# Kernel optimization log

Measured on AMD Instinct MI355X. Metric: run time of the kernel, lower is better.

The kernel has to match this reference:

```python
import jax, jax.numpy as jnp
import numpy as np


def setup_inputs() -> dict:
    key = jax.random.key(0)
    kq, kk, kv = jax.random.split(key, 3)
    B, S, D = 32, 2048, 64  # (batch*heads, seq_len, head_dim)
    q = jax.random.normal(kq, (B, S, D), dtype=jnp.float32)
    k = jax.random.normal(kk, (B, S, D), dtype=jnp.float32)
    v = jax.random.normal(kv, (B, S, D), dtype=jnp.float32)
    return {"q": q, "k": k, "v": v}


def reference(q, k, v):
    # attention = q @ k^T  (no scale, no mask: defaults scale=None, attn_mask=None)
    scores = jnp.einsum("bqd,bkd->bqk", q, k)  # [B, S, S] materialized, as in source
    attn = jax.nn.softmax(scores, axis=2)      # Softmax(dim=2) == key axis for 3D
    # dropout is identity in eval / deterministic reference
    return jnp.einsum("bqk,bkd->bqd", attn, v)
```

## Files before the change

kernel.cpp:

```cpp
#include <hip/hip_runtime.h>
#include <stdint.h>

typedef __attribute__((ext_vector_type(4)))  float    f32x4;
typedef __attribute__((ext_vector_type(16))) float    f32x16;
typedef __attribute__((ext_vector_type(8)))  _Float16 f16x8;
typedef __attribute__((ext_vector_type(8)))  __bf16   bf16x8;

#define SEQ   2048
#define DH    64
#define BQ    128
#define BK    64
#define NT    (SEQ / BK)
#define ROWE  72
#define TILEE (64 * ROWE)
#define L2E   1.44269504088896340736f

#if __has_builtin(__builtin_amdgcn_exp2f)
static __device__ __forceinline__ float fast_exp2(float x) { return __builtin_amdgcn_exp2f(x); }
#else
static __device__ __forceinline__ float fast_exp2(float x) {
  float r; asm("v_exp_f32 %0, %1" : "=v"(r) : "v"(x)); return r;
}
#endif
static __device__ __forceinline__ uint32_t pack2_bf16(float a, float b) {
  union { __bf16 h[2]; uint32_t u; } cv;
  cv.h[0] = (__bf16)a; cv.h[1] = (__bf16)b;
  return cv.u;
}
union frag_u { uint32_t u[4]; bf16x8 v; };

typedef const __attribute__((address_space(1))) uint32_t* gp1_t;
typedef __attribute__((address_space(3))) uint32_t*       lp3_t;

__host__ __device__ inline int sigma32(int m) {
  int b = m & 3, h = (m >> 2) & 1, c = m >> 3;
  return ((c & 1) << 4) | (h << 3) | ((c >> 1) << 2) | b;
}

__global__ __launch_bounds__(256)
void prepass(const float* __restrict__ K, const float* __restrict__ V,
             _Float16* __restrict__ Kh, __bf16* __restrict__ Vh) {
  const int blk = blockIdx.x;
  const int tid = threadIdx.x;
  if (blk < 32 * NT) {
    const float* src = K + ((size_t)(blk >> 5) * SEQ + (size_t)(blk & 31) * 64) * DH;
    _Float16*    dst = Kh + (size_t)blk * TILEE;
    const int row = tid >> 2, c = (tid & 3) << 4;
    const int srow = (row & 32) | sigma32(row & 31);
    const float* sp = src + srow * DH + c;
    f32x4 x0 = *(const f32x4*)(sp + 0),  x1 = *(const f32x4*)(sp + 4);
    f32x4 x2 = *(const f32x4*)(sp + 8),  x3 = *(const f32x4*)(sp + 12);
    f16x8 h0, h1;
#pragma unroll
    for (int j = 0; j < 4; ++j) {
      h0[j] = (_Float16)x0[j]; h0[j + 4] = (_Float16)x1[j];
      h1[j] = (_Float16)x2[j]; h1[j + 4] = (_Float16)x3[j];
    }
    *(f16x8*)(dst + row * ROWE + c)     = h0;
    *(f16x8*)(dst + row * ROWE + c + 8) = h1;
  } else {
    const int blk2 = blk - 32 * NT;
    const float* src = V + ((size_t)(blk2 >> 5) * SEQ + (size_t)(blk2 & 31) * 64) * DH;
    __bf16*      dst = Vh + (size_t)blk2 * TILEE;
#pragma unroll
    for (int it = 0; it < 4; ++it) {
      int task = tid + it * 256;
      int d = task & 63, g = task >> 6;
      const float* sp = src + (size_t)(4 * g) * DH + d;
      __bf16 hv[4];
#pragma unroll
      for (int j = 0; j < 4; ++j) hv[j] = (__bf16)sp[(size_t)j * DH];
      *(uint64_t*)(dst + d * ROWE + 4 * g) = *(uint64_t*)hv;
    }
  }
}

__global__ __launch_bounds__(256, 2)
void flash_attn_v10(const float* __restrict__ Q, const _Float16* __restrict__ Kh,
                    const __bf16* __restrict__ Vh, float* __restrict__ O) {
  __shared__ _Float16 Ksb[2][64][ROWE];
  __shared__ __bf16   Vtb[2][64][ROWE];
  __shared__ float    Ls[4][32];

  const int tid  = threadIdx.x;
  const int wv   = tid >> 6;
  const int lane = tid & 63;
  const int hfw  = lane >> 5;
  const int l31  = lane & 31;

  const int batch = blockIdx.x & 31;
  const int qblk  = blockIdx.x >> 5;

  const float* Qb = Q + (size_t)batch * SEQ * DH;
  float*       Ob = O + (size_t)batch * SEQ * DH;
  const uint32_t* Kt0 = (const uint32_t*)(Kh + (size_t)batch * NT * TILEE);
  const uint32_t* Vt0 = (const uint32_t*)(Vh + (size_t)batch * NT * TILEE);

  auto stageK = [&](int t, int buf) {
    const uint32_t* kgp = Kt0 + (size_t)t * (TILEE / 2);
    lp3_t kl = (lp3_t)&Ksb[buf][0][0];
#pragma unroll
    for (int j = wv; j < 9; j += 4)
      __builtin_amdgcn_global_load_lds((gp1_t)(kgp + j * 256 + lane * 4), kl + j * 256, 16, 0, 0);
  };
  auto stageV = [&](int t, int buf) {
    const uint32_t* vgp = Vt0 + (size_t)t * (TILEE / 2);
    lp3_t vl = (lp3_t)&Vtb[buf][0][0];
#pragma unroll
    for (int j = wv; j < 9; j += 4)
      __builtin_amdgcn_global_load_lds((gp1_t)(vgp + j * 256 + lane * 4), vl + j * 256, 16, 0, 0);
  };

  const int qrow = qblk * BQ + wv * 32 + l31;
  f16x8 qf[4];
  {
    const float* qp = Qb + (size_t)qrow * DH + hfw * 8;
#pragma unroll
    for (int ks = 0; ks < 4; ++ks) {
      f32x4 a = *(const f32x4*)(qp + ks * 16);
      f32x4 b = *(const f32x4*)(qp + ks * 16 + 4);
#pragma unroll
      for (int j = 0; j < 4; ++j) {
        qf[ks][j]     = (_Float16)(a[j] * L2E);
        qf[ks][j + 4] = (_Float16)(b[j] * L2E);
      }
    }
  }

  f32x16 acc0 = {}, acc1 = {};
  float lsum = 0.f;

  auto qk = [&](int buf, f32x16& s0, f32x16& s1) {
    s0 = {}; s1 = {};
#pragma unroll
    for (int ks = 0; ks < 4; ++ks) {
      const int dof = ks * 16 + hfw * 8;
      f16x8 kf0 = *(const f16x8*)&Ksb[buf][l31][dof];
      f16x8 kf1 = *(const f16x8*)&Ksb[buf][l31 + 32][dof];
      s0 = __builtin_amdgcn_mfma_f32_32x32x16_f16(kf0, qf[ks], s0, 0, 0, 0);
      s1 = __builtin_amdgcn_mfma_f32_32x32x16_f16(kf1, qf[ks], s1, 0, 0, 0);
    }
  };

  auto step = [&](int i, f32x16& c0, f32x16& c1, f32x16& n0, f32x16& n1) {
    __syncthreads();
    if (i + 2 < NT) stageK(i + 2, i & 1);
    if (i + 1 < NT) stageV(i + 1, (i + 1) & 1);
    __builtin_amdgcn_s_setprio(1);

    if (i + 1 < NT) qk((i + 1) & 1, n0, n1);

    frag_u fr[4];
#pragma unroll
    for (int t2 = 0; t2 < 2; ++t2) {
      const f32x16& s = t2 ? c1 : c0;
      float p[16];
#pragma unroll
      for (int j = 0; j < 16; ++j) p[j] = fast_exp2(s[j]);
      float a0 = (p[0] + p[1]) + (p[2] + p[3]);
      float a1 = (p[4] + p[5]) + (p[6] + p[7]);
      float a2 = (p[8] + p[9]) + (p[10] + p[11]);
      float a3 = (p[12] + p[13]) + (p[14] + p[15]);
      lsum += (a0 + a1) + (a2 + a3);
      fr[2 * t2    ].u[0] = pack2_bf16(p[0],  p[1]);
      fr[2 * t2    ].u[1] = pack2_bf16(p[2],  p[3]);
      fr[2 * t2    ].u[2] = pack2_bf16(p[8],  p[9]);
      fr[2 * t2    ].u[3] = pack2_bf16(p[10], p[11]);
      fr[2 * t2 + 1].u[0] = pack2_bf16(p[4],  p[5]);
      fr[2 * t2 + 1].u[1] = pack2_bf16(p[6],  p[7]);
      fr[2 * t2 + 1].u[2] = pack2_bf16(p[12], p[13]);
      fr[2 * t2 + 1].u[3] = pack2_bf16(p[14], p[15]);
    }

    const int vb = i & 1;
#pragma unroll
    for (int ks = 0; ks < 4; ++ks) {
      const int kof = ks * 16 + hfw * 8;
      bf16x8 v0 = *(const bf16x8*)&Vtb[vb][l31][kof];
      bf16x8 v1 = *(const bf16x8*)&Vtb[vb][l31 + 32][kof];
      acc0 = __builtin_amdgcn_mfma_f32_32x32x16_bf16(fr[ks].v, v0, acc0, 0, 0, 0);
      acc1 = __builtin_amdgcn_mfma_f32_32x32x16_bf16(fr[ks].v, v1, acc1, 0, 0, 0);
    }
    __builtin_amdgcn_s_setprio(0);
  };

  stageK(0, 0); stageV(0, 0); stageK(1, 1);
  __syncthreads();
  f32x16 sA0, sA1, sB0, sB1;
  qk(0, sA0, sA1);

#pragma unroll 1
  for (int i = 0; i < NT; i += 2) {
    step(i,     sA0, sA1, sB0, sB1);
    step(i + 1, sB0, sB1, sA0, sA1);
  }

  float tot = lsum + __shfl_xor(lsum, 32);
  Ls[wv][l31] = __builtin_amdgcn_rcpf(tot);
#pragma unroll
  for (int j = 0; j < 16; ++j) {
    int row = (j & 3) + 8 * (j >> 2) + 4 * hfw;
    float inv = Ls[wv][row];
    size_t off = (size_t)(qblk * BQ + wv * 32 + row) * DH + l31;
    Ob[off]      = acc0[j] * inv;
    Ob[off + 32] = acc1[j] * inv;
  }
}

extern "C" void kernel_launch(void* const* d_in, const int* in_sizes, int n_in,
                              void* d_out, int out_size, void* d_ws, size_t ws_size,
                              hipStream_t stream) {
  (void)in_sizes; (void)n_in; (void)ws_size; (void)out_size;
  const float* q = (const float*)d_in[0];
  const float* k = (const float*)d_in[1];
  const float* v = (const float*)d_in[2];
  float* o = (float*)d_out;
  _Float16* Kh = (_Float16*)d_ws;
  __bf16*   Vh = (__bf16*)((char*)d_ws + (size_t)32 * NT * TILEE * sizeof(_Float16));

  prepass<<<dim3(2 * 32 * NT), dim3(256), 0, stream>>>(k, v, Kh, Vh);
  flash_attn_v10<<<dim3(32 * (SEQ / BQ)), dim3(256), 0, stream>>>(q, Kh, Vh, o);
}
```

Baseline: 138.6 us.

## Split key range across two warp groups per block with LDS reduction

Blocks grow to 512 threads: each of the four query warps is paired with a second warp that handles the second half of the key tiles (split-K within a block). The two halves keep their own double-buffered K/V tiles in LDS, and their partial outputs and row sums are combined through shared memory at the end. The software pipeline that overlapped the next tile's QK with the current tile's PV is dropped in favour of a simpler loop with setprio hints. The aim is more waves per CU to hide latency, at the cost of doubled LDS use, a final reduction, and less overlap inside each wave.

```diff
diff --git a/kernel.cpp b/kernel.cpp
--- a/kernel.cpp
+++ b/kernel.cpp
@@ -11,6 +11,7 @@
 #define BQ    128
 #define BK    64
 #define NT    (SEQ / BK)
+#define HNT   (NT / 2)
 #define ROWE  72
 #define TILEE (64 * ROWE)
 #define L2E   1.44269504088896340736f
@@ -75,15 +76,17 @@
   }
 }
 
-__global__ __launch_bounds__(256, 2)
-void flash_attn_v10(const float* __restrict__ Q, const _Float16* __restrict__ Kh,
+__global__ __launch_bounds__(512, 2)
+void flash_attn_v16(const float* __restrict__ Q, const _Float16* __restrict__ Kh,
                     const __bf16* __restrict__ Vh, float* __restrict__ O) {
-  __shared__ _Float16 Ksb[2][64][ROWE];
-  __shared__ __bf16   Vtb[2][64][ROWE];
+  __shared__ _Float16 Ksb[2][2][64][ROWE];
+  __shared__ __bf16   Vtb[2][2][64][ROWE];
   __shared__ float    Ls[4][32];
 
   const int tid  = threadIdx.x;
   const int wv   = tid >> 6;
+  const int qw   = wv & 3;
+  const int kh   = wv >> 2;
   const int lane = tid & 63;
   const int hfw  = lane >> 5;
   const int l31  = lane & 31;
@@ -96,22 +99,19 @@
   const uint32_t* Kt0 = (const uint32_t*)(Kh + (size_t)batch * NT * TILEE);
   const uint32_t* Vt0 = (const uint32_t*)(Vh + (size_t)batch * NT * TILEE);
 
-  auto stageK = [&](int t, int buf) {
+  auto stage = [&](int t, int buf) {
     const uint32_t* kgp = Kt0 + (size_t)t * (TILEE / 2);
-    lp3_t kl = (lp3_t)&Ksb[buf][0][0];
-#pragma unroll
-    for (int j = wv; j < 9; j += 4)
+    const uint32_t* vgp = Vt0 + (size_t)t * (TILEE / 2);
+    lp3_t kl = (lp3_t)&Ksb[kh][buf][0][0];
+    lp3_t vl = (lp3_t)&Vtb[kh][buf][0][0];
+#pragma unroll
+    for (int j = qw; j < 9; j += 4) {
       __builtin_amdgcn_global_load_lds((gp1_t)(kgp + j * 256 + lane * 4), kl + j * 256, 16, 0, 0);
+      __builtin_amdgcn_global_load_lds((gp1_t)(vgp + j * 256 + lane * 4), vl + j * 256, 16, 0, 0);
+    }
   };
-  auto stageV = [&](int t, int buf) {
-    const uint32_t* vgp = Vt0 + (size_t)t * (TILEE / 2);
-    lp3_t vl = (lp3_t)&Vtb[buf][0][0];
-#pragma unroll
-    for (int j = wv; j < 9; j += 4)
-      __builtin_amdgcn_global_load_lds((gp1_t)(vgp + j * 256 + lane * 4), vl + j * 256, 16, 0, 0);
-  };
-
-  const int qrow = qblk * BQ + wv * 32 + l31;
+
+  const int qrow = qblk * BQ + qw * 32 + l31;
   f16x8 qf[4];
   {
     const float* qp = Qb + (size_t)qrow * DH + hfw * 8;
@@ -130,30 +130,31 @@
   f32x16 acc0 = {}, acc1 = {};
   float lsum = 0.f;
 
-  auto qk = [&](int buf, f32x16& s0, f32x16& s1) {
-    s0 = {}; s1 = {};
+  const int t0 = kh * HNT;
+  stage(t0, 0);
+
+#pragma unroll 1
+  for (int li = 0; li < HNT; ++li) {
+    __syncthreads();
+    if (li + 1 < HNT) stage(t0 + li + 1, (li + 1) & 1);
+    const int buf = li & 1;
+
+    __builtin_amdgcn_s_setprio(1);
+    f32x16 s0 = {}, s1 = {};
 #pragma unroll
     for (int ks = 0; ks < 4; ++ks) {
-      const int dof = ks * 16 + hfw * 8;
-      f16x8 kf0 = *(const f16x8*)&Ksb[buf][l31][dof];
-      f16x8 kf1 = *(const f16x8*)&Ksb[buf][l31 + 32][dof];
+      int dof = ks * 16 + hfw * 8;
+      f16x8 kf0 = *(const f16x8*)&Ksb[kh][buf][l31][dof];
+      f16x8 kf1 = *(const f16x8*)&Ksb[kh][buf][l31 + 32][dof];
       s0 = __builtin_amdgcn_mfma_f32_32x32x16_f16(kf0, qf[ks], s0, 0, 0, 0);
       s1 = __builtin_amdgcn_mfma_f32_32x32x16_f16(kf1, qf[ks], s1, 0, 0, 0);
     }
-  };
-
-  auto step = [&](int i, f32x16& c0, f32x16& c1, f32x16& n0, f32x16& n1) {
-    __syncthreads();
-    if (i + 2 < NT) stageK(i + 2, i & 1);
-    if (i + 1 < NT) stageV(i + 1, (i + 1) & 1);
-    __builtin_amdgcn_s_setprio(1);
-
-    if (i + 1 < NT) qk((i + 1) & 1, n0, n1);
+    __builtin_amdgcn_s_setprio(0);
 
     frag_u fr[4];
 #pragma unroll
     for (int t2 = 0; t2 < 2; ++t2) {
-      const f32x16& s = t2 ? c1 : c0;
+      const f32x16& s = t2 ? s1 : s0;
       float p[16];
 #pragma unroll
       for (int j = 0; j < 16; ++j) p[j] = fast_exp2(s[j]);
@@ -172,38 +173,49 @@
       fr[2 * t2 + 1].u[3] = pack2_bf16(p[14], p[15]);
     }
 
-    const int vb = i & 1;
+    __builtin_amdgcn_s_setprio(1);
 #pragma unroll
     for (int ks = 0; ks < 4; ++ks) {
-      const int kof = ks * 16 + hfw * 8;
-      bf16x8 v0 = *(const bf16x8*)&Vtb[vb][l31][kof];
-      bf16x8 v1 = *(const bf16x8*)&Vtb[vb][l31 + 32][kof];
+      int kof = ks * 16 + hfw * 8;
+      bf16x8 v0 = *(const bf16x8*)&Vtb[kh][buf][l31][kof];
+      bf16x8 v1 = *(const bf16x8*)&Vtb[kh][buf][l31 + 32][kof];
       acc0 = __builtin_amdgcn_mfma_f32_32x32x16_bf16(fr[ks].v, v0, acc0, 0, 0, 0);
       acc1 = __builtin_amdgcn_mfma_f32_32x32x16_bf16(fr[ks].v, v1, acc1, 0, 0, 0);
     }
     __builtin_amdgcn_s_setprio(0);
-  };
-
-  stageK(0, 0); stageV(0, 0); stageK(1, 1);
+  }
+
+  float tot = lsum + __shfl_xor(lsum, 32);
   __syncthreads();
-  f32x16 sA0, sA1, sB0, sB1;
-  qk(0, sA0, sA1);
-
-#pragma unroll 1
-  for (int i = 0; i < NT; i += 2) {
-    step(i,     sA0, sA1, sB0, sB1);
-    step(i + 1, sB0, sB1, sA0, sA1);
-  }
-
-  float tot = lsum + __shfl_xor(lsum, 32);
-  Ls[wv][l31] = __builtin_amdgcn_rcpf(tot);
-#pragma unroll
-  for (int j = 0; j < 16; ++j) {
-    int row = (j & 3) + 8 * (j >> 2) + 4 * hfw;
-    float inv = Ls[wv][row];
-    size_t off = (size_t)(qblk * BQ + wv * 32 + row) * DH + l31;
-    Ob[off]      = acc0[j] * inv;
-    Ob[off + 32] = acc1[j] * inv;
+  float* cb = (float*)&Ksb[0][0][0][0];
+  float* sb = (float*)&Vtb[0][0][0][0];
+  if (kh == 1) {
+    const int base = (qw * 64 + lane) * 33;
+#pragma unroll
+    for (int j = 0; j < 16; ++j) {
+      cb[base + j]      = acc0[j];
+      cb[base + j + 16] = acc1[j];
+    }
+    sb[qw * 64 + lane] = tot;
+  }
+  __syncthreads();
+  if (kh == 0) {
+    const int base = (qw * 64 + lane) * 33;
+    float tot2 = tot + sb[qw * 64 + lane];
+    Ls[qw][l31] = __builtin_amdgcn_rcpf(tot2);
+#pragma unroll
+    for (int j = 0; j < 16; ++j) {
+      acc0[j] += cb[base + j];
+      acc1[j] += cb[base + j + 16];
+    }
+#pragma unroll
+    for (int j = 0; j < 16; ++j) {
+      int row = (j & 3) + 8 * (j >> 2) + 4 * hfw;
+      float inv = Ls[qw][row];
+      size_t off = (size_t)(qblk * BQ + qw * 32 + row) * DH + l31;
+      Ob[off]      = acc0[j] * inv;
+      Ob[off + 32] = acc1[j] * inv;
+    }
   }
 }
 
@@ -219,5 +231,5 @@
   __bf16*   Vh = (__bf16*)((char*)d_ws + (size_t)32 * NT * TILEE * sizeof(_Float16));
 
   prepass<<<dim3(2 * 32 * NT), dim3(256), 0, stream>>>(k, v, Kh, Vh);
-  flash_attn_v10<<<dim3(32 * (SEQ / BQ)), dim3(256), 0, stream>>>(q, Kh, Vh, o);
-}
+  flash_attn_v16<<<dim3(32 * (SEQ / BQ)), dim3(512), 0, stream>>>(q, Kh, Vh, o);
+}
```

Result: no change. 139.5 us (+0.7%).
